# Kernel optimization log

Hardware: AMD Instinct MI355X
Metric: run time of the kernel (lower is better)

Reference implementation:

```python
import jax, jax.numpy as jnp
import numpy as np

N, NPG, BS = 32000, 1000, 32
E, H, L, R, K = 512000, 128, 3, 8, 64


def setup_inputs() -> dict:
    key = jax.random.key(0)
    ks = jax.random.split(key, 16)
    sc = 0.05
    x = jax.random.normal(ks[0], (N, H), jnp.float32)
    W_rel = jax.random.normal(ks[1], (L, R, H, H), jnp.float32) * sc
    W_self = jax.random.normal(ks[2], (L, H, H), jnp.float32) * sc
    rel_table = jax.random.normal(ks[3], (R, H), jnp.float32)
    Zn = jax.random.normal(ks[4], (K, H), jnp.float32) * sc
    proj_W = jax.random.normal(ks[5], (L * H, H), jnp.float32) * sc
    proj_b = jnp.zeros((H,), jnp.float32)
    fc_W = jax.random.normal(ks[6], (2 * L * H + 2 * H, 1), jnp.float32) * sc
    fc_b = jnp.zeros((1,), jnp.float32)
    rep_seq = jax.random.normal(ks[7], (BS, H), jnp.float32)
    src = jax.random.randint(ks[8], (E,), 0, N, jnp.int32)
    dst = jax.random.randint(ks[9], (E,), 0, N, jnp.int32)
    etype = jax.random.randint(ks[10], (E,), 0, R, jnp.int32)
    graph_id = (jnp.arange(N, dtype=jnp.int32) // NPG).astype(jnp.int32)
    head_ids = (jnp.arange(BS, dtype=jnp.int32) * NPG)           # node with id==1 per subgraph
    tail_ids = (jnp.arange(BS, dtype=jnp.int32) * NPG + 1)       # node with id==2 per subgraph
    rel_labels = jax.random.randint(ks[11], (BS,), 0, R, jnp.int32)
    return dict(x=x, W_rel=W_rel, W_self=W_self, rel_table=rel_table, Zn=Zn,
                proj_W=proj_W, proj_b=proj_b, fc_W=fc_W, fc_b=fc_b, rep_seq=rep_seq,
                src=src, dst=dst, etype=etype, graph_id=graph_id,
                head_ids=head_ids, tail_ids=tail_ids, rel_labels=rel_labels)


def reference(x, W_rel, W_self, rel_table, Zn, proj_W, proj_b, fc_W, fc_b, rep_seq,
              src, dst, etype, graph_id, head_ids, tail_ids, rel_labels):
    n, h_dim = x.shape
    bs = head_ids.shape[0]
    # RGCN message passing: aggregate src features per (dst, rel), then per-rel linear.
    seg = dst.astype(jnp.int32) * R + etype.astype(jnp.int32)  # [E]
    h = x
    reprs = []
    for l in range(L):
        agg = jax.ops.segment_sum(h[src], seg, num_segments=n * R)  # [N*R, H]
        agg = agg.reshape(n, R, h_dim)
        msg = jnp.einsum('nri,rio->no', agg, W_rel[l])
        h = jax.nn.relu(msg + h @ W_self[l])
        reprs.append(h)
    repr_ = jnp.stack(reprs, axis=1)  # [N, L, H]
    # mean_nodes pooling per subgraph
    counts = jax.ops.segment_sum(jnp.ones((n,), x.dtype), graph_id, num_segments=bs)
    g_mean = jax.ops.segment_sum(repr_, graph_id, num_segments=bs) / counts[:, None, None]
    g_out = jax.nn.leaky_relu(g_mean.reshape(bs, L * h_dim) @ proj_W + proj_b)  # [bs, H]
    # head/tail gathers
    head_flat = repr_[head_ids].reshape(bs, L * h_dim)
    tail_flat = repr_[tail_ids].reshape(bs, L * h_dim)
    rel_embs = rel_table[rel_labels]  # [bs, H]
    h_out = head_flat @ proj_W + proj_b
    t_out = tail_flat @ proj_W + proj_b
    # community view: cluster assignment (softmax) then summary (sigmoid)
    s1 = jax.nn.sigmoid(jax.nn.softmax(h_out @ Zn.T, axis=-1) @ Zn)
    s2 = jax.nn.sigmoid(jax.nn.softmax(t_out @ Zn.T, axis=-1) @ Zn)
    s = s1 * s2
    # view attention aggregation over [subgraph, sequence, community] views
    views = jnp.stack([g_out, rep_seq, s], axis=1)  # [bs, 3, H]
    att = jax.nn.softmax(jnp.sum(rel_embs[:, None, :] * views, axis=-1), axis=-1)  # [bs, 3]
    view_aggr = jnp.sum(att[:, :, None] * views, axis=1)  # [bs, H]
    # positive triplet scoring
    g_rep = jnp.concatenate([head_flat, tail_flat, rel_embs, view_aggr], axis=1)
    out_pos = g_rep @ fc_W + fc_b  # [bs, 1]
    return out_pos
```

## Files before the change

### kernel.cpp

```cpp
#include <hip/hip_runtime.h>

#define N_NODES 32000
#define NPG     1000
#define BSZ     32
#define NEDGE   512000
#define H       128
#define NL      3
#define NR      8
#define NKK     1152
#define NKA     1024
#define NBIN2   262144

typedef __attribute__((ext_vector_type(8))) short short8;
typedef __attribute__((ext_vector_type(4))) float float4v;

__device__ __forceinline__ float bf2f(unsigned short u) {
  union { unsigned int i; float f; } v;
  v.i = ((unsigned int)u) << 16;
  return v.f;
}
__device__ __forceinline__ unsigned short f2bf(float f) {
  union { float f; unsigned int i; } v;
  v.f = f;
  unsigned int x = v.i;
  return (unsigned short)((x + 0x7FFFu + ((x >> 16) & 1u)) >> 16);
}

__device__ __forceinline__ void gl_lds16(const void* g, void* l) {
  __builtin_amdgcn_global_load_lds((__attribute__((address_space(1))) void*)g,
                                   (__attribute__((address_space(3))) void*)l,
                                   16, 0, 0);
}

__global__ __launch_bounds__(256) void k_prep(
    const float* __restrict__ x, const int* __restrict__ dst,
    const int* __restrict__ etype, const int* __restrict__ graph_id,
    unsigned short* __restrict__ hb, int* __restrict__ cnt, int* __restrict__ gcount)
{
  const int b = blockIdx.x, t = threadIdx.x;
  if (b < 4000) {
    const size_t i = ((size_t)b * 256 + t) * 4;
    float4 v = *(const float4*)(x + i);
    ushort4 u = { f2bf(v.x), f2bf(v.y), f2bf(v.z), f2bf(v.w) };
    *(ushort4*)(hb + i) = u;
  } else if (b < 6000) {
    const int e = (b - 4000) * 256 + t;
    atomicAdd(&cnt[dst[e] * 8 + etype[e]], 1);
  } else {
    __shared__ int hist[BSZ];
    if (t < BSZ) hist[t] = 0;
    __syncthreads();
    const int n = (b - 6000) * 256 + t;
    if (n < N_NODES) atomicAdd(&hist[graph_id[n]], 1);
    __syncthreads();
    if (t < BSZ) { int v = hist[t]; if (v) atomicAdd(&gcount[t], v); }
  }
}

__global__ __launch_bounds__(256) void k_wt(
    const float* __restrict__ W_rel, const float* __restrict__ W_self,
    unsigned short* __restrict__ Bt)
{
  __shared__ unsigned short T[128 * 137];
  const int t = threadIdx.x;
  const int l = blockIdx.x / 9, rr = blockIdx.x % 9;
  const float* src = (rr < 8) ? W_rel + ((size_t)l * NR + rr) * H * H
                              : W_self + (size_t)l * H * H;
  #pragma unroll
  for (int ph = 0; ph < 16; ++ph) {
    const int i  = ph * 8 + (t >> 5);
    const int o4 = (t & 31) * 4;
    float4 v = *(const float4*)(src + (size_t)i * H + o4);
    T[(o4 + 0) * 137 + i] = f2bf(v.x);
    T[(o4 + 1) * 137 + i] = f2bf(v.y);
    T[(o4 + 2) * 137 + i] = f2bf(v.z);
    T[(o4 + 3) * 137 + i] = f2bf(v.w);
  }
  __syncthreads();
  #pragma unroll
  for (int ph = 0; ph < 16; ++ph) {
    const int o  = ph * 8 + (t >> 5);
    const int i4 = (t & 31) * 4;
    ushort4 u = { T[o * 137 + i4], T[o * 137 + i4 + 1],
                  T[o * 137 + i4 + 2], T[o * 137 + i4 + 3] };
    *(ushort4*)(Bt + (size_t)l * (H * NKK) + (size_t)o * NKK + rr * 128 + i4) = u;
  }
}

__global__ __launch_bounds__(256) void k_scanA(const int* __restrict__ cnt,
                                               int* __restrict__ bsum) {
  __shared__ int red[256];
  const int t = threadIdx.x;
  int4 v = *(const int4*)(cnt + blockIdx.x * 1024 + t * 4);
  red[t] = v.x + v.y + v.z + v.w;
  __syncthreads();
  for (int off = 128; off > 0; off >>= 1) {
    if (t < off) red[t] += red[t + off];
    __syncthreads();
  }
  if (t == 0) bsum[blockIdx.x] = red[0];
}

__global__ __launch_bounds__(256) void k_scanC(const int* __restrict__ cnt,
                                               const int* __restrict__ bsum,
                                               int* __restrict__ row_ptr2,
                                               int* __restrict__ cursor) {
  __shared__ int ts[256], bsx[256];
  const int t = threadIdx.x;
  const int base = blockIdx.x * 1024 + t * 4;
  int4 v = *(const int4*)(cnt + base);
  const int s = v.x + v.y + v.z + v.w;
  ts[t]  = s;
  bsx[t] = bsum[t];
  __syncthreads();
  for (int off = 1; off < 256; off <<= 1) {
    int a = (t >= off) ? ts[t - off]  : 0;
    int c = (t >= off) ? bsx[t - off] : 0;
    __syncthreads();
    ts[t] += a; bsx[t] += c;
    __syncthreads();
  }
  const int boff = (blockIdx.x == 0) ? 0 : bsx[blockIdx.x - 1];
  int ex = ts[t] - s + boff;
  int4 w = { ex, ex + v.x, ex + v.x + v.y, ex + v.x + v.y + v.z };
  *(int4*)(row_ptr2 + base) = w;
  *(int4*)(cursor + base) = w;
}

__global__ void k_fill(const int* __restrict__ src, const int* __restrict__ dst,
                       const int* __restrict__ etype, int* __restrict__ cursor,
                       int* __restrict__ edge_off) {
  int e = blockIdx.x * blockDim.x + threadIdx.x;
  if (e < NEDGE) {
    int p = atomicAdd(&cursor[dst[e] * 8 + etype[e]], 1);
    edge_off[p] = src[e];
  }
}

__global__ __launch_bounds__(256) void k_agg(
    const unsigned short* __restrict__ Hin,
    const int* __restrict__ row_ptr2,
    const int* __restrict__ edge_off,
    unsigned short* __restrict__ A)
{
  const int tid = threadIdx.x;
  const int j  = tid >> 5;
  const int li = tid & 31;
  const int p  = li >> 4;
  const int q  = li & 15;
  const int n  = blockIdx.x;
  const uint4* H4 = (const uint4*)Hin;
  const int b = row_ptr2[n * 8 + j];
  const int e = row_ptr2[n * 8 + j + 1];
  float acc[8] = {0.f, 0.f, 0.f, 0.f, 0.f, 0.f, 0.f, 0.f};
#define ACC8(u, ok) { \
    const unsigned int xx = (ok) ? (u).x : 0u, yy = (ok) ? (u).y : 0u; \
    const unsigned int zz = (ok) ? (u).z : 0u, ww = (ok) ? (u).w : 0u; \
    acc[0] += bf2f((unsigned short)(xx & 0xffff)); \
    acc[1] += bf2f((unsigned short)(xx >> 16));    \
    acc[2] += bf2f((unsigned short)(yy & 0xffff)); \
    acc[3] += bf2f((unsigned short)(yy >> 16));    \
    acc[4] += bf2f((unsigned short)(zz & 0xffff)); \
    acc[5] += bf2f((unsigned short)(zz >> 16));    \
    acc[6] += bf2f((unsigned short)(ww & 0xffff)); \
    acc[7] += bf2f((unsigned short)(ww >> 16)); }
  for (int k = b + p; k < e; k += 4) {
    const int k1 = k + 2;
    const bool v1 = k1 < e;
    const int o0 = edge_off[k];
    const int o1 = edge_off[v1 ? k1 : k];
    uint4 u0 = H4[(size_t)o0 * 16 + q];
    uint4 u1 = H4[(size_t)o1 * 16 + q];
    ACC8(u0, true)
    ACC8(u1, v1)
  }
#undef ACC8
  #pragma unroll
  for (int i = 0; i < 8; ++i) acc[i] += __shfl_xor(acc[i], 16);
  if (p == 0) {
    uint4 w;
    w.x = (unsigned int)f2bf(acc[0]) | ((unsigned int)f2bf(acc[1]) << 16);
    w.y = (unsigned int)f2bf(acc[2]) | ((unsigned int)f2bf(acc[3]) << 16);
    w.z = (unsigned int)f2bf(acc[4]) | ((unsigned int)f2bf(acc[5]) << 16);
    w.w = (unsigned int)f2bf(acc[6]) | ((unsigned int)f2bf(acc[7]) << 16);
    *(uint4*)(A + (size_t)n * NKA + j * H + q * 8) = w;
  }
}

__global__ __launch_bounds__(256, 3) void k_gemmA(
    const unsigned short* __restrict__ Ag,
    const unsigned short* __restrict__ Bg,
    const unsigned short* __restrict__ Hin,
    unsigned short* __restrict__ Hout,
    float* __restrict__ gmean, int layer)
{
  __shared__ __align__(16) unsigned short pool[24576];
  const int tid = threadIdx.x;
  const int w = tid >> 6, lane = tid & 63;
  const int l15 = lane & 15, quad = lane >> 4;
  const int m0 = blockIdx.x * 64;
  const int rbase = (w & 1) * 32;
  const int cbase = (w >> 1) * 64;

  float4v acc[2][4];
  #pragma unroll
  for (int i = 0; i < 2; ++i)
    #pragma unroll
    for (int jj = 0; jj < 4; ++jj) acc[i][jj] = (float4v){0.f, 0.f, 0.f, 0.f};

  auto stageA = [&](unsigned short* dstL, const int kb) {
    #pragma unroll
    for (int rep = 0; rep < 2; ++rep) {
      const int g = rep * 256 + tid, row = g >> 3, c = g & 7;
      const unsigned short* srcp = (kb < NKA)
          ? Ag  + (size_t)(m0 + row) * NKA + kb + ((c ^ (row & 7)) * 8)
          : Hin + (size_t)(m0 + row) * H + (kb - NKA) + ((c ^ (row & 7)) * 8);
      gl_lds16(srcp, dstL + (size_t)g * 8);
    }
  };
  auto stageB = [&](unsigned short* dstL, const int kb) {
    #pragma unroll
    for (int rep = 0; rep < 4; ++rep) {
      const int g = rep * 256 + tid, row = g >> 3, c = g & 7;
      gl_lds16(Bg + (size_t)row * NKK + kb + ((c ^ (row & 7)) * 8), dstL + (size_t)g * 8);
    }
  };
  auto compute = [&](const unsigned short* ac, const unsigned short* bc) {
    #pragma unroll
    for (int s = 0; s < 2; ++s) {
      const int c = s * 4 + quad;
      short8 af[2], bfv[4];
      #pragma unroll
      for (int i = 0; i < 2; ++i) {
        const int row = rbase + i * 16 + l15;
        af[i] = *(const short8*)(ac + row * 64 + ((c ^ (row & 7)) * 8));
      }
      #pragma unroll
      for (int jj = 0; jj < 4; ++jj) {
        const int orow = cbase + jj * 16 + l15;
        bfv[jj] = *(const short8*)(bc + orow * 64 + ((c ^ (orow & 7)) * 8));
      }
      #pragma unroll
      for (int i = 0; i < 2; ++i)
        #pragma unroll
        for (int jj = 0; jj < 4; ++jj)
          acc[i][jj] = __builtin_amdgcn_mfma_f32_16x16x32_bf16(af[i], bfv[jj], acc[i][jj], 0, 0, 0);
    }
  };

  stageA(pool, 0);
  stageB(pool + 4096, 0);
  asm volatile("s_waitcnt vmcnt(0)" ::: "memory");
  __builtin_amdgcn_s_barrier();
  __builtin_amdgcn_sched_barrier(0);

  #pragma unroll 2
  for (int kt = 0; kt < 17; ++kt) {
    const int cur = kt & 1;
    const unsigned short* ac = pool + (cur ? 12288 : 0);
    const unsigned short* bc = pool + (cur ? 16384 : 4096);
    const int kb = (kt + 1) * 64;
    stageA(pool + (cur ? 0 : 12288), kb);
    stageB(pool + (cur ? 4096 : 16384), kb);
    asm volatile("s_waitcnt vmcnt(6)" ::: "memory");
    __builtin_amdgcn_s_barrier();
    __builtin_amdgcn_sched_barrier(0);
    compute(ac, bc);
    __builtin_amdgcn_sched_barrier(0);
    __builtin_amdgcn_s_barrier();
  }
  asm volatile("s_waitcnt vmcnt(0)" ::: "memory");
  __builtin_amdgcn_s_barrier();
  __builtin_amdgcn_sched_barrier(0);
  compute(pool + 12288, pool + 16384);
  __syncthreads();

  #pragma unroll
  for (int i = 0; i < 2; ++i)
    #pragma unroll
    for (int jj = 0; jj < 4; ++jj)
      #pragma unroll
      for (int r = 0; r < 4; ++r) {
        const int row = rbase + i * 16 + quad * 4 + r;
        const int col = cbase + jj * 16 + l15;
        pool[row * 136 + col] = f2bf(fmaxf(acc[i][jj][r], 0.f));
      }
  __syncthreads();
  #pragma unroll
  for (int rep = 0; rep < 4; ++rep) {
    const int g = rep * 256 + tid;
    const int row = g >> 4, c = g & 15;
    *(uint4*)(Hout + (size_t)(m0 + row) * H + c * 8) = *(const uint4*)(pool + row * 136 + c * 8);
  }

  const int g0 = m0 / NPG;
  const int bnd = (g0 + 1) * NPG - m0;
  if (tid < H) {
    float s0 = 0.f, s1 = 0.f;
    #pragma unroll 8
    for (int r2 = 0; r2 < 64; ++r2) {
      float v = bf2f(pool[r2 * 136 + tid]);
      if (r2 < bnd) s0 += v; else s1 += v;
    }
    atomicAdd(&gmean[(size_t)g0 * (NL * H) + layer * H + tid], s0);
    if (bnd < 64)
      atomicAdd(&gmean[(size_t)(g0 + 1) * (NL * H) + layer * H + tid], s1);
  }
}

__global__ __launch_bounds__(128) void k_final(
    const unsigned short* __restrict__ hb, const float* __restrict__ gmean,
    const int* __restrict__ gcount,
    const float* __restrict__ rel_tb, const float* __restrict__ Zn,
    const float* __restrict__ projW, const float* __restrict__ projB,
    const float* __restrict__ fcW, const float* __restrict__ fcB,
    const float* __restrict__ repSeq,
    const int* __restrict__ head_ids, const int* __restrict__ tail_ids,
    const int* __restrict__ rel_lab, float* __restrict__ out)
{
  const int b = blockIdx.x;
  const int o = threadIdx.x;
  __shared__ float gm[384], hf[384], tf[384];
  __shared__ float go[128], ho[128], t_o[128], re[128], rs[128], sv[128];
  __shared__ float lg[128], pr[128], red[128], att[3];

  const int hid = head_ids[b], tlid = tail_ids[b], rl = rel_lab[b];
  const float cinv = 1.f / (float)gcount[b];
  #pragma unroll
  for (int l = 0; l < NL; ++l) {
    gm[l * H + o] = gmean[(size_t)b * (NL * H) + l * H + o] * cinv;
    hf[l * H + o] = bf2f(hb[((size_t)(l + 1) * N_NODES + hid) * H + o]);
    tf[l * H + o] = bf2f(hb[((size_t)(l + 1) * N_NODES + tlid) * H + o]);
  }
  re[o] = rel_tb[rl * H + o];
  rs[o] = repSeq[b * H + o];
  __syncthreads();

  float pb = projB[o];
  float sg = pb, sh = pb, st = pb;
  for (int i = 0; i < NL * H; ++i) {
    float wv = projW[i * H + o];
    sg = fmaf(gm[i], wv, sg);
    sh = fmaf(hf[i], wv, sh);
    st = fmaf(tf[i], wv, st);
  }
  go[o] = (sg > 0.f) ? sg : 0.01f * sg;
  ho[o] = sh;
  t_o[o] = st;
  __syncthreads();

  {
    const int k = o & 63;
    const float* v = (o < 64) ? ho : t_o;
    float s = 0.f;
    for (int i = 0; i < H; ++i) s = fmaf(v[i], Zn[k * H + i], s);
    lg[o] = s;
  }
  __syncthreads();
  if (o < 2) {
    float* l0 = &lg[o * 64];
    float* p0 = &pr[o * 64];
    float mx = l0[0];
    for (int k = 1; k < 64; ++k) mx = fmaxf(mx, l0[k]);
    float sum = 0.f;
    for (int k = 0; k < 64; ++k) { float e = __expf(l0[k] - mx); p0[k] = e; sum += e; }
    float inv = 1.f / sum;
    for (int k = 0; k < 64; ++k) p0[k] *= inv;
  }
  __syncthreads();
  {
    float s1 = 0.f, s2 = 0.f;
    for (int k = 0; k < 64; ++k) {
      float z = Zn[k * H + o];
      s1 = fmaf(pr[k], z, s1);
      s2 = fmaf(pr[64 + k], z, s2);
    }
    s1 = 1.f / (1.f + __expf(-s1));
    s2 = 1.f / (1.f + __expf(-s2));
    sv[o] = s1 * s2;
  }
  __syncthreads();
  if (o == 0) {
    float d0 = 0.f, d1 = 0.f, d2 = 0.f;
    for (int i = 0; i < H; ++i) { d0 += re[i] * go[i]; d1 += re[i] * rs[i]; d2 += re[i] * sv[i]; }
    float mx = fmaxf(d0, fmaxf(d1, d2));
    float e0 = __expf(d0 - mx), e1 = __expf(d1 - mx), e2 = __expf(d2 - mx);
    float inv = 1.f / (e0 + e1 + e2);
    att[0] = e0 * inv; att[1] = e1 * inv; att[2] = e2 * inv;
  }
  __syncthreads();
  float va = att[0] * go[o] + att[1] * rs[o] + att[2] * sv[o];

  float p = 0.f;
  p = fmaf(hf[o],       fcW[o],       p);
  p = fmaf(hf[128 + o], fcW[128 + o], p);
  p = fmaf(hf[256 + o], fcW[256 + o], p);
  p = fmaf(tf[o],       fcW[384 + o], p);
  p = fmaf(tf[128 + o], fcW[512 + o], p);
  p = fmaf(tf[256 + o], fcW[640 + o], p);
  p = fmaf(re[o],       fcW[768 + o], p);
  p = fmaf(va,          fcW[896 + o], p);
  red[o] = p;
  __syncthreads();
  if (o == 0) {
    float s = 0.f;
    for (int i = 0; i < 128; ++i) s += red[i];
    out[b] = s + fcB[0];
  }
}

extern "C" void kernel_launch(void* const* d_in, const int* in_sizes, int n_in,
                              void* d_out, int out_size, void* d_ws, size_t ws_size,
                              hipStream_t stream) {
  const float* x        = (const float*)d_in[0];
  const float* W_rel    = (const float*)d_in[1];
  const float* W_self   = (const float*)d_in[2];
  const float* rel_tb   = (const float*)d_in[3];
  const float* Zn       = (const float*)d_in[4];
  const float* proj_W   = (const float*)d_in[5];
  const float* proj_b   = (const float*)d_in[6];
  const float* fc_W     = (const float*)d_in[7];
  const float* fc_b     = (const float*)d_in[8];
  const float* rep_seq  = (const float*)d_in[9];
  const int* src      = (const int*)d_in[10];
  const int* dst      = (const int*)d_in[11];
  const int* etype    = (const int*)d_in[12];
  const int* graph_id = (const int*)d_in[13];
  const int* head_ids = (const int*)d_in[14];
  const int* tail_ids = (const int*)d_in[15];
  const int* rel_lab  = (const int*)d_in[16];
  float* out = (float*)d_out;

  char* w = (char*)d_ws;
  unsigned short* A   = (unsigned short*)w; w += (size_t)N_NODES * NKA * 2;
  unsigned short* hb  = (unsigned short*)w; w += (size_t)(NL + 1) * N_NODES * H * 2;
  unsigned short* Bt2 = (unsigned short*)w; w += (size_t)NL * H * NKK * 2;
  int* row_ptr2 = (int*)w;  w += (size_t)(NBIN2 + 8) * 4;
  int* cursor   = (int*)w;  w += (size_t)NBIN2 * 4;
  int* edge_off = (int*)w;  w += (size_t)NEDGE * 4;
  int* bsum     = (int*)w;  w += (size_t)256 * 4;
  char* z = w;
  int* cnt     = (int*)w;   w += (size_t)NBIN2 * 4;
  int* gcount  = (int*)w;   w += (size_t)32 * 4;
  float* gmean = (float*)w; w += (size_t)BSZ * NL * H * 4;
  size_t zbytes = (size_t)(w - z);

  hipMemsetAsync(z, 0, zbytes, stream);
  k_prep <<<6125, 256, 0, stream>>>(x, dst, etype, graph_id, hb, cnt, gcount);
  k_wt   <<<27, 256, 0, stream>>>(W_rel, W_self, Bt2);
  k_scanA<<<NBIN2 / 1024, 256, 0, stream>>>(cnt, bsum);
  k_scanC<<<NBIN2 / 1024, 256, 0, stream>>>(cnt, bsum, row_ptr2, cursor);
  k_fill <<<NEDGE / 256, 256, 0, stream>>>(src, dst, etype, cursor, edge_off);

  for (int l = 0; l < NL; ++l) {
    const unsigned short* hp = hb + (size_t)l * N_NODES * H;
    unsigned short* hn = hb + (size_t)(l + 1) * N_NODES * H;
    k_agg  <<<N_NODES, 256, 0, stream>>>(hp, row_ptr2, edge_off, A);
    k_gemmA<<<N_NODES / 64, 256, 0, stream>>>(A, Bt2 + (size_t)l * H * NKK, hp, hn, gmean, l);
  }
  k_final<<<BSZ, H, 0, stream>>>(hb, gmean, gcount, rel_tb, Zn, proj_W, proj_b, fc_W, fc_b,
                                 rep_seq, head_ids, tail_ids, rel_lab, out);
  (void)in_sizes; (void)n_in; (void)out_size; (void)ws_size;
}
```

Measured before the change: 331.7 us.

## Load A operand directly into registers, keep only B in LDS

The gemm kernel now fetches the A tile (aggregated features and previous hidden state) straight from global memory into registers in MFMA fragment layout, double-buffered in registers, instead of staging it through LDS. Only the weight tile B stays in LDS, which shrinks shared memory from 48KB to 32KB and allows the launch bound to rise to 4 blocks per CU. This cuts LDS traffic and frees space for more occupancy, but the register-direct A loads are less coalesced (16-byte per-lane row strides) and the tighter launch bound may pressure registers. The vmcnt wait count assumes the exact number of outstanding loads per step.

```diff
diff --git a/kernel.cpp b/kernel.cpp
--- a/kernel.cpp
+++ b/kernel.cpp
@@ -187,14 +187,14 @@
   }
 }
 
-__global__ __launch_bounds__(256, 3) void k_gemmA(
+__global__ __launch_bounds__(256, 4) void k_gemmA(
     const unsigned short* __restrict__ Ag,
     const unsigned short* __restrict__ Bg,
     const unsigned short* __restrict__ Hin,
     unsigned short* __restrict__ Hout,
     float* __restrict__ gmean, int layer)
 {
-  __shared__ __align__(16) unsigned short pool[24576];
+  __shared__ __align__(16) unsigned short lbuf[2][8192];
   const int tid = threadIdx.x;
   const int w = tid >> 6, lane = tid & 63;
   const int l15 = lane & 15, quad = lane >> 4;
@@ -208,14 +208,24 @@
     #pragma unroll
     for (int jj = 0; jj < 4; ++jj) acc[i][jj] = (float4v){0.f, 0.f, 0.f, 0.f};
 
-  auto stageA = [&](unsigned short* dstL, const int kb) {
-    #pragma unroll
-    for (int rep = 0; rep < 2; ++rep) {
-      const int g = rep * 256 + tid, row = g >> 3, c = g & 7;
-      const unsigned short* srcp = (kb < NKA)
-          ? Ag  + (size_t)(m0 + row) * NKA + kb + ((c ^ (row & 7)) * 8)
-          : Hin + (size_t)(m0 + row) * H + (kb - NKA) + ((c ^ (row & 7)) * 8);
-      gl_lds16(srcp, dstL + (size_t)g * 8);
+  const unsigned short* a0base = Ag + (size_t)(m0 + rbase + l15) * NKA + quad * 8;
+  const unsigned short* a1base = Ag + (size_t)(m0 + rbase + 16 + l15) * NKA + quad * 8;
+  const unsigned short* h0base = Hin + (size_t)(m0 + rbase + l15) * H + quad * 8;
+  const unsigned short* h1base = Hin + (size_t)(m0 + rbase + 16 + l15) * H + quad * 8;
+
+  auto loadA = [&](short8 dst[2][2], const int kt) {
+    if (kt < 16) {
+      const int kb = kt * 64;
+      dst[0][0] = *(const short8*)(a0base + kb);
+      dst[0][1] = *(const short8*)(a0base + kb + 32);
+      dst[1][0] = *(const short8*)(a1base + kb);
+      dst[1][1] = *(const short8*)(a1base + kb + 32);
+    } else {
+      const int cb = (kt - 16) * 64;
+      dst[0][0] = *(const short8*)(h0base + cb);
+      dst[0][1] = *(const short8*)(h0base + cb + 32);
+      dst[1][0] = *(const short8*)(h1base + cb);
+      dst[1][1] = *(const short8*)(h1base + cb + 32);
     }
   };
   auto stageB = [&](unsigned short* dstL, const int kb) {
@@ -225,16 +235,11 @@
       gl_lds16(Bg + (size_t)row * NKK + kb + ((c ^ (row & 7)) * 8), dstL + (size_t)g * 8);
     }
   };
-  auto compute = [&](const unsigned short* ac, const unsigned short* bc) {
+  auto compute = [&](const short8 a[2][2], const unsigned short* bc) {
     #pragma unroll
     for (int s = 0; s < 2; ++s) {
       const int c = s * 4 + quad;
-      short8 af[2], bfv[4];
-      #pragma unroll
-      for (int i = 0; i < 2; ++i) {
-        const int row = rbase + i * 16 + l15;
-        af[i] = *(const short8*)(ac + row * 64 + ((c ^ (row & 7)) * 8));
-      }
+      short8 bfv[4];
       #pragma unroll
       for (int jj = 0; jj < 4; ++jj) {
         const int orow = cbase + jj * 16 + l15;
@@ -244,37 +249,39 @@
       for (int i = 0; i < 2; ++i)
         #pragma unroll
         for (int jj = 0; jj < 4; ++jj)
-          acc[i][jj] = __builtin_amdgcn_mfma_f32_16x16x32_bf16(af[i], bfv[jj], acc[i][jj], 0, 0, 0);
+          acc[i][jj] = __builtin_amdgcn_mfma_f32_16x16x32_bf16(a[i][s], bfv[jj], acc[i][jj], 0, 0, 0);
     }
   };
 
-  stageA(pool, 0);
-  stageB(pool + 4096, 0);
-  asm volatile("s_waitcnt vmcnt(0)" ::: "memory");
-  __builtin_amdgcn_s_barrier();
-  __builtin_amdgcn_sched_barrier(0);
-
-  #pragma unroll 2
-  for (int kt = 0; kt < 17; ++kt) {
-    const int cur = kt & 1;
-    const unsigned short* ac = pool + (cur ? 12288 : 0);
-    const unsigned short* bc = pool + (cur ? 16384 : 4096);
-    const int kb = (kt + 1) * 64;
-    stageA(pool + (cur ? 0 : 12288), kb);
-    stageB(pool + (cur ? 4096 : 16384), kb);
-    asm volatile("s_waitcnt vmcnt(6)" ::: "memory");
-    __builtin_amdgcn_s_barrier();
-    __builtin_amdgcn_sched_barrier(0);
-    compute(ac, bc);
-    __builtin_amdgcn_sched_barrier(0);
-    __builtin_amdgcn_s_barrier();
-  }
-  asm volatile("s_waitcnt vmcnt(0)" ::: "memory");
-  __builtin_amdgcn_s_barrier();
-  __builtin_amdgcn_sched_barrier(0);
-  compute(pool + 12288, pool + 16384);
-  __syncthreads();
-
+  short8 aE[2][2], aO[2][2];
+
+  loadA(aE, 0);
+  stageB(lbuf[0], 0);
+
+#define STEP(KT, AIN, AOUT, BCUR, BNXT)                                 \
+  {                                                                     \
+    if ((KT) + 1 < 18) {                                                \
+      loadA(AOUT, (KT) + 1);                                            \
+      stageB(lbuf[BNXT], ((KT) + 1) * 64);                              \
+      asm volatile("s_waitcnt vmcnt(8)" ::: "memory");                  \
+    } else {                                                            \
+      asm volatile("s_waitcnt vmcnt(0)" ::: "memory");                  \
+    }                                                                   \
+    __builtin_amdgcn_s_barrier();                                       \
+    __builtin_amdgcn_sched_barrier(0);                                  \
+    compute(AIN, lbuf[BCUR]);                                           \
+    __builtin_amdgcn_sched_barrier(0);                                  \
+    __builtin_amdgcn_s_barrier();                                       \
+  }
+
+  for (int kt2 = 0; kt2 < 18; kt2 += 2) {
+    STEP(kt2,     aE, aO, 0, 1);
+    STEP(kt2 + 1, aO, aE, 1, 0);
+  }
+#undef STEP
+  __syncthreads();
+
+  unsigned short* pool = &lbuf[0][0];
   #pragma unroll
   for (int i = 0; i < 2; ++i)
     #pragma unroll
```

After: 366.9 us. 10.6% more time.
